# Performance work log

Hardware: AMD Instinct MI355X
Metric: run time of the kernel (lower is better)

The kernel has to match this reference:

```python
import jax, jax.numpy as jnp
import numpy as np

B, NQ, NK, DQ, DK, DV, H = 4, 512, 512, 512, 512, 512, 128
NEG_INF = -1e20


def setup_inputs() -> dict:
    key = jax.random.key(0)
    ks = jax.random.split(key, 7)
    Q = jax.random.normal(ks[0], (B, NQ, DQ), dtype=jnp.float32)
    K = jax.random.normal(ks[1], (B, NK, DK), dtype=jnp.float32)
    V = jax.random.normal(ks[2], (B, NK, DV), dtype=jnp.float32)
    # learned params (LazyLinear, bias=False): y = x @ W with W[in, out]
    Wq = jax.random.normal(ks[3], (DQ, H), dtype=jnp.float32) / np.sqrt(DQ)
    Wk = jax.random.normal(ks[4], (DK, H), dtype=jnp.float32) / np.sqrt(DK)
    wv = jax.random.normal(ks[5], (H,), dtype=jnp.float32) / np.sqrt(H)
    valid_lens = jax.random.randint(ks[6], (B,), 1, NK + 1).astype(jnp.int64)
    return {"Q": Q, "K": K, "V": V, "Wq": Wq, "Wk": Wk, "wv": wv,
            "valid_lens": valid_lens}


def reference(Q, K, V, Wq, Wk, wv, valid_lens):
    # Project queries and keys to shared hidden size H
    Qp = Q @ Wq                      # (B, NQ, H)
    Kp = K @ Wk                      # (B, NK, H)
    # Additive (Bahdanau) broadcast: (B, NQ, NK, H)
    S = jnp.tanh(Qp[:, :, None, :] + Kp[:, None, :, :])
    # Linear score to scalar: (B, NQ, NK)
    scores = jnp.einsum('bqkh,h->bqk', S, wv)
    # Mask positions k >= valid_lens[b] (1-D valid_lens broadcast over queries)
    kv_idx = jnp.arange(scores.shape[-1])[None, None, :]
    mask = kv_idx < valid_lens[:, None, None]
    scores = jnp.where(mask, scores, NEG_INF)
    W = jax.nn.softmax(scores, axis=-1)  # dropout rate 0.0 -> identity
    return jnp.einsum('bqk,bkv->bqv', W, V)
```

## Files before the change

### kernel.cpp

```cpp
#include <hip/hip_runtime.h>

#define B_   4
#define NQ_  512
#define NK_  512
#define D_   512
#define H_   128

typedef __attribute__((ext_vector_type(8))) short short8;
typedef __attribute__((ext_vector_type(4))) float f32x4;

__device__ __forceinline__ float fexp2(float x) { return __builtin_amdgcn_exp2f(x); }
__device__ __forceinline__ float frcp(float x)  { return __builtin_amdgcn_rcpf(x); }
__device__ __forceinline__ unsigned short f2bf(float f) {
    unsigned int u = __builtin_bit_cast(unsigned int, f);
    u += 0x7FFFu + ((u >> 16) & 1u);
    return (unsigned short)(u >> 16);
}

#define WS_QKP   0
#define WS_PP    524288
#define WS_WP    4718592
#define WS_WBF   4718848
#define WS_VT    5243136

__global__ __launch_bounds__(256) void proj_kernel(
    const float* __restrict__ Q, const float* __restrict__ K,
    const float* __restrict__ Wq, const float* __restrict__ Wk,
    float* __restrict__ Pp)
{
    const int xb = blockIdx.x;
    const int ks = blockIdx.y;
    const bool isQ = xb < 16;
    const float* __restrict__ X = isQ ? Q : K;
    const float* __restrict__ W = isQ ? Wq : Wk;
    const int r0 = (xb & 15) * 128;
    const int k0 = ks * 64;
    const int t  = threadIdx.x;

    __shared__ float At[32][132];
    __shared__ float Wl[32][132];

    const int cg = t & 15;
    const int rg = t >> 4;
    float acc[8][8] = {};

    for (int kc = 0; kc < 2; ++kc) {
        if (kc) __syncthreads();
        #pragma unroll
        for (int p = 0; p < 4; ++p) {
            const int idx = p * 256 + t;
            const int row = idx & 127;
            const int kq  = (idx >> 7) * 4;
            const float4 v = *reinterpret_cast<const float4*>(
                X + (size_t)(r0 + row) * D_ + k0 + kc * 32 + kq);
            At[kq + 0][row] = v.x; At[kq + 1][row] = v.y;
            At[kq + 2][row] = v.z; At[kq + 3][row] = v.w;
        }
        #pragma unroll
        for (int p = 0; p < 4; ++p) {
            const int idx = p * 256 + t;
            const int kr  = idx >> 5;
            const int c4  = (idx & 31) * 4;
            *reinterpret_cast<float4*>(&Wl[kr][c4]) =
                *reinterpret_cast<const float4*>(
                    W + (size_t)(k0 + kc * 32 + kr) * H_ + c4);
        }
        __syncthreads();

        #pragma unroll 4
        for (int k = 0; k < 32; ++k) {
            const float4 a0 = *reinterpret_cast<const float4*>(&At[k][rg * 8]);
            const float4 a1 = *reinterpret_cast<const float4*>(&At[k][rg * 8 + 4]);
            const float4 b0 = *reinterpret_cast<const float4*>(&Wl[k][cg * 4]);
            const float4 b1 = *reinterpret_cast<const float4*>(&Wl[k][64 + cg * 4]);
            const float aa[8] = {a0.x, a0.y, a0.z, a0.w, a1.x, a1.y, a1.z, a1.w};
            const float bb[8] = {b0.x, b0.y, b0.z, b0.w, b1.x, b1.y, b1.z, b1.w};
            #pragma unroll
            for (int r = 0; r < 8; ++r)
                #pragma unroll
                for (int c = 0; c < 8; ++c)
                    acc[r][c] = fmaf(aa[r], bb[c], acc[r][c]);
        }
    }

    float* __restrict__ dst = Pp + (size_t)ks * (4096 * 128);
    #pragma unroll
    for (int r = 0; r < 8; ++r) {
        const int grow = xb * 128 + rg * 8 + r;
        *reinterpret_cast<float4*>(dst + (size_t)grow * H_ + cg * 4) =
            make_float4(acc[r][0], acc[r][1], acc[r][2], acc[r][3]);
        *reinterpret_cast<float4*>(dst + (size_t)grow * H_ + 64 + cg * 4) =
            make_float4(acc[r][4], acc[r][5], acc[r][6], acc[r][7]);
    }
}

__global__ __launch_bounds__(256) void proj_add_kernel(
    const float* __restrict__ Pp, const float* __restrict__ wv,
    float* __restrict__ QKp, float* __restrict__ wp)
{
    const int i = blockIdx.x * 256 + threadIdx.x;
    const float C2 = 2.88539008177792681472f;
    float4 s = make_float4(0.f, 0.f, 0.f, 0.f);
    #pragma unroll
    for (int p = 0; p < 8; ++p) {
        const float4 v = reinterpret_cast<const float4*>(Pp)[(size_t)p * 131072 + i];
        s.x += v.x; s.y += v.y; s.z += v.z; s.w += v.w;
    }
    s.x *= C2; s.y *= C2; s.z *= C2; s.w *= C2;
    reinterpret_cast<float4*>(QKp)[i] = s;

    if (blockIdx.x == 0 && threadIdx.x < 64) {
        const float2 w2 = reinterpret_cast<const float2*>(wv)[threadIdx.x];
        const float wn0 = -2.0f * w2.x;
        const float wn1 = -2.0f * w2.y;
        reinterpret_cast<float4*>(wp)[threadIdx.x] =
            make_float4(wn0, wn1, wn0 + wn1, 0.0f);
    }
}

__global__ __launch_bounds__(256) void transposeV_kernel(
    const float* __restrict__ V, unsigned short* __restrict__ Vt)
{
    const int kt = blockIdx.x, dt = blockIdx.y, b = blockIdx.z;
    const int t  = threadIdx.x;
    __shared__ float Vl[64][69];

    #pragma unroll
    for (int p = 0; p < 4; ++p) {
        const int idx = p * 256 + t;
        const int r  = idx >> 4;
        const int c4 = (idx & 15) * 4;
        const float4 v = *reinterpret_cast<const float4*>(
            V + ((size_t)b * NK_ + kt * 64 + r) * D_ + dt * 64 + c4);
        Vl[r][c4 + 0] = v.x; Vl[r][c4 + 1] = v.y;
        Vl[r][c4 + 2] = v.z; Vl[r][c4 + 3] = v.w;
    }
    __syncthreads();

    #pragma unroll
    for (int p = 0; p < 4; ++p) {
        const int idx = p * 256 + t;
        const int d  = idx >> 4;
        const int k4 = (idx & 15) * 4;
        ushort4 o;
        o.x = f2bf(Vl[k4 + 0][d]); o.y = f2bf(Vl[k4 + 1][d]);
        o.z = f2bf(Vl[k4 + 2][d]); o.w = f2bf(Vl[k4 + 3][d]);
        *reinterpret_cast<ushort4*>(
            Vt + ((size_t)b * D_ + dt * 64 + d) * NK_ + kt * 64 + k4) = o;
    }
}

__global__ __launch_bounds__(512) void score_softmax_kernel(
    const float* __restrict__ QKp, const float* __restrict__ wp,
    const int* __restrict__ valid_lens, unsigned short* __restrict__ Wbf)
{
    const int b  = blockIdx.y;
    const int q0 = blockIdx.x * 8;
    const int t  = threadIdx.x;
    const int w    = __builtin_amdgcn_readfirstlane(t >> 6);
    const int lane = t & 63;

    __shared__ __align__(16) float4 Ks[64][33];

    const float4* __restrict__ Q4 =
        reinterpret_cast<const float4*>(QKp + (size_t)(b * NQ_ + q0 + w) * H_);
    const float4* __restrict__ wp4 = reinterpret_cast<const float4*>(wp);
    const float4* __restrict__ Kp4 =
        reinterpret_cast<const float4*>(QKp + (size_t)(2048 + b * NK_) * H_);

    float vals[8];

    for (int c = 0; c < 8; ++c) {
        if (c) __syncthreads();
        #pragma unroll
        for (int p = 0; p < 4; ++p) {
            const int idx = p * 512 + t;
            const int r   = idx >> 5;
            const int h4  = idx & 31;
            Ks[r][h4] = Kp4[(size_t)(c * 64 + r) * 32 + h4];
        }
        __syncthreads();

        float s = 0.0f;
        #pragma unroll 8
        for (int g = 0; g < 32; ++g) {
            const float4 kv = Ks[lane][g];
            const float4 qa = Q4[g];
            const float4 wa = wp4[2 * g];
            const float4 wb = wp4[2 * g + 1];
            const float e0 = fexp2(qa.x + kv.x);
            const float e1 = fexp2(qa.y + kv.y);
            const float e2 = fexp2(qa.z + kv.z);
            const float e3 = fexp2(qa.w + kv.w);
            float n0 = fmaf(wa.x, e1, wa.z); n0 = fmaf(wa.y, e0, n0);
            float n1 = fmaf(wb.x, e3, wb.z); n1 = fmaf(wb.y, e2, n1);
            const float d0 = (1.0f + e0) * (1.0f + e1);
            const float d1 = (1.0f + e2) * (1.0f + e3);
            s = fmaf(n0, frcp(d0), s);
            s = fmaf(n1, frcp(d1), s);
        }
        vals[c] = s;
    }

    const int vl = valid_lens[b];
    float m = -1e30f;
    #pragma unroll
    for (int c = 0; c < 8; ++c) {
        const int k = c * 64 + lane;
        vals[c] = (k < vl) ? vals[c] : -1e30f;
        m = fmaxf(m, vals[c]);
    }
    #pragma unroll
    for (int off = 32; off >= 1; off >>= 1)
        m = fmaxf(m, __shfl_xor(m, off, 64));

    const float L2E = 1.44269504088896340736f;
    float e[8];
    float sum = 0.0f;
    #pragma unroll
    for (int c = 0; c < 8; ++c) {
        e[c] = fexp2((vals[c] - m) * L2E);
        sum += e[c];
    }
    #pragma unroll
    for (int off = 32; off >= 1; off >>= 1)
        sum += __shfl_xor(sum, off, 64);

    const float inv = frcp(sum);
    unsigned short* __restrict__ dst = Wbf + (size_t)(b * NQ_ + q0 + w) * NK_;
    #pragma unroll
    for (int c = 0; c < 8; ++c)
        dst[c * 64 + lane] = f2bf(e[c] * inv);
}

__global__ __launch_bounds__(256) void av_gemm_kernel(
    const unsigned short* __restrict__ Wbf, const unsigned short* __restrict__ Vt,
    float* __restrict__ O)
{
    const int c0 = blockIdx.x * 64;
    const int r0 = blockIdx.y * 64;
    const int b  = blockIdx.z;
    const int t  = threadIdx.x;
    const int wave = __builtin_amdgcn_readfirstlane(t >> 6);
    const int lane = t & 63;
    const int m    = lane & 15;
    const int quad = lane >> 4;

    __shared__ unsigned short Al [64][136];
    __shared__ unsigned short Btl[64][136];

    f32x4 acc0 = {0.f,0.f,0.f,0.f}, acc1 = {0.f,0.f,0.f,0.f};
    f32x4 acc2 = {0.f,0.f,0.f,0.f}, acc3 = {0.f,0.f,0.f,0.f};

    for (int kc = 0; kc < 4; ++kc) {
        if (kc) __syncthreads();
        #pragma unroll
        for (int p = 0; p < 4; ++p) {
            const int idx = p * 256 + t;
            const int rl = idx >> 4;
            const int k8 = (idx & 15) * 8;
            *reinterpret_cast<uint4*>(&Al[rl][k8]) =
                *reinterpret_cast<const uint4*>(
                    Wbf + ((size_t)b * NQ_ + r0 + rl) * NK_ + kc * 128 + k8);
            *reinterpret_cast<uint4*>(&Btl[rl][k8]) =
                *reinterpret_cast<const uint4*>(
                    Vt + ((size_t)b * D_ + c0 + rl) * NK_ + kc * 128 + k8);
        }
        __syncthreads();

        #pragma unroll
        for (int sub = 0; sub < 4; ++sub) {
            const int kcol = sub * 32 + quad * 8;
            const short8 a = *reinterpret_cast<const short8*>(&Al[wave * 16 + m][kcol]);
            const short8 b0 = *reinterpret_cast<const short8*>(&Btl[ 0 + m][kcol]);
            const short8 b1 = *reinterpret_cast<const short8*>(&Btl[16 + m][kcol]);
            const short8 b2 = *reinterpret_cast<const short8*>(&Btl[32 + m][kcol]);
            const short8 b3 = *reinterpret_cast<const short8*>(&Btl[48 + m][kcol]);
            acc0 = __builtin_amdgcn_mfma_f32_16x16x32_bf16(a, b0, acc0, 0, 0, 0);
            acc1 = __builtin_amdgcn_mfma_f32_16x16x32_bf16(a, b1, acc1, 0, 0, 0);
            acc2 = __builtin_amdgcn_mfma_f32_16x16x32_bf16(a, b2, acc2, 0, 0, 0);
            acc3 = __builtin_amdgcn_mfma_f32_16x16x32_bf16(a, b3, acc3, 0, 0, 0);
        }
    }

    const size_t rowbase = (size_t)b * NQ_ + r0 + wave * 16 + quad * 4;
    #pragma unroll
    for (int i = 0; i < 4; ++i) {
        float* __restrict__ orow = O + (rowbase + i) * D_ + c0 + m;
        orow[ 0] = acc0[i];
        orow[16] = acc1[i];
        orow[32] = acc2[i];
        orow[48] = acc3[i];
    }
}

extern "C" void kernel_launch(void* const* d_in, const int* in_sizes, int n_in,
                              void* d_out, int out_size, void* d_ws, size_t ws_size,
                              hipStream_t stream) {
    (void)in_sizes; (void)n_in; (void)out_size; (void)ws_size;

    const float* Q   = (const float*)d_in[0];
    const float* K   = (const float*)d_in[1];
    const float* V   = (const float*)d_in[2];
    const float* Wq  = (const float*)d_in[3];
    const float* Wk  = (const float*)d_in[4];
    const float* wv  = (const float*)d_in[5];
    const int*   vl  = (const int*)d_in[6];
    float* out = (float*)d_out;

    float* ws  = (float*)d_ws;
    float* QKp = ws + WS_QKP;
    float* Pp  = ws + WS_PP;
    float* wp  = ws + WS_WP;
    unsigned short* Wbf = (unsigned short*)(ws + WS_WBF);
    unsigned short* Vt  = (unsigned short*)(ws + WS_VT);

    proj_kernel<<<dim3(32, 8), 256, 0, stream>>>(Q, K, Wq, Wk, Pp);
    proj_add_kernel<<<dim3(512), 256, 0, stream>>>(Pp, wv, QKp, wp);
    transposeV_kernel<<<dim3(8, 8, 4), 256, 0, stream>>>(V, Vt);
    score_softmax_kernel<<<dim3(64, 4), 512, 0, stream>>>(QKp, wp, vl, Wbf);
    av_gemm_kernel<<<dim3(8, 8, 4), 256, 0, stream>>>(Wbf, Vt, out);
}
```

Baseline: 131.4 us.

## Precompute exponentials of projections, merge V transpose into projection, split score rows

The projection-add stage now stores exp2 of the scaled projections, so the score loop replaces per-element exp2 with multiplies, using exp(a+b)=exp(a)exp(b) and one reciprocal per pair. The V transpose is folded into the projection kernel as extra blocks, removing one launch. The score kernel splits each query row across two waves (4 rows per block, 512 blocks) and combines the softmax max and sum through shared memory. This adds occupancy but risks overflow or precision loss when exp of large projections is multiplied.

```diff
diff --git a/kernel.cpp b/kernel.cpp
--- a/kernel.cpp
+++ b/kernel.cpp
@@ -17,86 +17,120 @@
     return (unsigned short)(u >> 16);
 }
 
-#define WS_QKP   0
+
+#define WS_EQK   0
 #define WS_PP    524288
 #define WS_WP    4718592
 #define WS_WBF   4718848
 #define WS_VT    5243136
 
-__global__ __launch_bounds__(256) void proj_kernel(
+__global__ __launch_bounds__(256) void prep_kernel(
     const float* __restrict__ Q, const float* __restrict__ K,
     const float* __restrict__ Wq, const float* __restrict__ Wk,
-    float* __restrict__ Pp)
+    const float* __restrict__ V,
+    float* __restrict__ Pp, unsigned short* __restrict__ Vt)
 {
-    const int xb = blockIdx.x;
-    const int ks = blockIdx.y;
-    const bool isQ = xb < 16;
-    const float* __restrict__ X = isQ ? Q : K;
-    const float* __restrict__ W = isQ ? Wq : Wk;
-    const int r0 = (xb & 15) * 128;
-    const int k0 = ks * 64;
-    const int t  = threadIdx.x;
-
-    __shared__ float At[32][132];
-    __shared__ float Wl[32][132];
-
-    const int cg = t & 15;
-    const int rg = t >> 4;
-    float acc[8][8] = {};
-
-    for (int kc = 0; kc < 2; ++kc) {
-        if (kc) __syncthreads();
+    __shared__ float smem[2 * 32 * 132];
+    const int t = threadIdx.x;
+
+    if (blockIdx.x < 32) {
+        const int xb = blockIdx.x;
+        const int ks = blockIdx.y;
+        const bool isQ = xb < 16;
+        const float* __restrict__ X = isQ ? Q : K;
+        const float* __restrict__ W = isQ ? Wq : Wk;
+        const int r0 = (xb & 15) * 128;
+        const int k0 = ks * 64;
+
+        float (*At)[132] = (float(*)[132])smem;
+        float (*Wl)[132] = (float(*)[132])(smem + 32 * 132);
+
+        const int cg = t & 15;
+        const int rg = t >> 4;
+        float acc[8][8] = {};
+
+        for (int kc = 0; kc < 2; ++kc) {
+            if (kc) __syncthreads();
+            #pragma unroll
+            for (int p = 0; p < 4; ++p) {
+                const int idx = p * 256 + t;
+                const int row = idx & 127;
+                const int kq  = (idx >> 7) * 4;
+                const float4 v = *reinterpret_cast<const float4*>(
+                    X + (size_t)(r0 + row) * D_ + k0 + kc * 32 + kq);
+                At[kq + 0][row] = v.x; At[kq + 1][row] = v.y;
+                At[kq + 2][row] = v.z; At[kq + 3][row] = v.w;
+            }
+            #pragma unroll
+            for (int p = 0; p < 4; ++p) {
+                const int idx = p * 256 + t;
+                const int kr  = idx >> 5;
+                const int c4  = (idx & 31) * 4;
+                *reinterpret_cast<float4*>(&Wl[kr][c4]) =
+                    *reinterpret_cast<const float4*>(
+                        W + (size_t)(k0 + kc * 32 + kr) * H_ + c4);
+            }
+            __syncthreads();
+
+            #pragma unroll 4
+            for (int k = 0; k < 32; ++k) {
+                const float4 a0 = *reinterpret_cast<const float4*>(&At[k][rg * 8]);
+                const float4 a1 = *reinterpret_cast<const float4*>(&At[k][rg * 8 + 4]);
+                const float4 b0 = *reinterpret_cast<const float4*>(&Wl[k][cg * 4]);
+                const float4 b1 = *reinterpret_cast<const float4*>(&Wl[k][64 + cg * 4]);
+                const float aa[8] = {a0.x, a0.y, a0.z, a0.w, a1.x, a1.y, a1.z, a1.w};
+                const float bb[8] = {b0.x, b0.y, b0.z, b0.w, b1.x, b1.y, b1.z, b1.w};
+                #pragma unroll
+                for (int r = 0; r < 8; ++r)
+                    #pragma unroll
+                    for (int c = 0; c < 8; ++c)
+                        acc[r][c] = fmaf(aa[r], bb[c], acc[r][c]);
+            }
+        }
+
+        float* __restrict__ dst = Pp + (size_t)blockIdx.y * (4096 * 128);
+        #pragma unroll
+        for (int r = 0; r < 8; ++r) {
+            const int grow = xb * 128 + rg * 8 + r;
+            *reinterpret_cast<float4*>(dst + (size_t)grow * H_ + cg * 4) =
+                make_float4(acc[r][0], acc[r][1], acc[r][2], acc[r][3]);
+            *reinterpret_cast<float4*>(dst + (size_t)grow * H_ + 64 + cg * 4) =
+                make_float4(acc[r][4], acc[r][5], acc[r][6], acc[r][7]);
+        }
+    } else {
+        const int id = (blockIdx.x - 32) * 8 + blockIdx.y;
+        const int kt = id & 7, dt = (id >> 3) & 7, b = id >> 6;
+        float (*Vl)[69] = (float(*)[69])smem;
+
         #pragma unroll
         for (int p = 0; p < 4; ++p) {
             const int idx = p * 256 + t;
-            const int row = idx & 127;
-            const int kq  = (idx >> 7) * 4;
+            const int r  = idx >> 4;
+            const int c4 = (idx & 15) * 4;
             const float4 v = *reinterpret_cast<const float4*>(
-                X + (size_t)(r0 + row) * D_ + k0 + kc * 32 + kq);
-            At[kq + 0][row] = v.x; At[kq + 1][row] = v.y;
-            At[kq + 2][row] = v.z; At[kq + 3][row] = v.w;
-        }
+                V + ((size_t)b * NK_ + kt * 64 + r) * D_ + dt * 64 + c4);
+            Vl[r][c4 + 0] = v.x; Vl[r][c4 + 1] = v.y;
+            Vl[r][c4 + 2] = v.z; Vl[r][c4 + 3] = v.w;
+        }
+        __syncthreads();
+
         #pragma unroll
         for (int p = 0; p < 4; ++p) {
             const int idx = p * 256 + t;
-            const int kr  = idx >> 5;
-            const int c4  = (idx & 31) * 4;
-            *reinterpret_cast<float4*>(&Wl[kr][c4]) =
-                *reinterpret_cast<const float4*>(
-                    W + (size_t)(k0 + kc * 32 + kr) * H_ + c4);
-        }
-        __syncthreads();
-
-        #pragma unroll 4
-        for (int k = 0; k < 32; ++k) {
-            const float4 a0 = *reinterpret_cast<const float4*>(&At[k][rg * 8]);
-            const float4 a1 = *reinterpret_cast<const float4*>(&At[k][rg * 8 + 4]);
-            const float4 b0 = *reinterpret_cast<const float4*>(&Wl[k][cg * 4]);
-            const float4 b1 = *reinterpret_cast<const float4*>(&Wl[k][64 + cg * 4]);
-            const float aa[8] = {a0.x, a0.y, a0.z, a0.w, a1.x, a1.y, a1.z, a1.w};
-            const float bb[8] = {b0.x, b0.y, b0.z, b0.w, b1.x, b1.y, b1.z, b1.w};
-            #pragma unroll
-            for (int r = 0; r < 8; ++r)
-                #pragma unroll
-                for (int c = 0; c < 8; ++c)
-                    acc[r][c] = fmaf(aa[r], bb[c], acc[r][c]);
-        }
-    }
-
-    float* __restrict__ dst = Pp + (size_t)ks * (4096 * 128);
-    #pragma unroll
-    for (int r = 0; r < 8; ++r) {
-        const int grow = xb * 128 + rg * 8 + r;
-        *reinterpret_cast<float4*>(dst + (size_t)grow * H_ + cg * 4) =
-            make_float4(acc[r][0], acc[r][1], acc[r][2], acc[r][3]);
-        *reinterpret_cast<float4*>(dst + (size_t)grow * H_ + 64 + cg * 4) =
-            make_float4(acc[r][4], acc[r][5], acc[r][6], acc[r][7]);
+            const int d  = idx >> 4;
+            const int k4 = (idx & 15) * 4;
+            ushort4 o;
+            o.x = f2bf(Vl[k4 + 0][d]); o.y = f2bf(Vl[k4 + 1][d]);
+            o.z = f2bf(Vl[k4 + 2][d]); o.w = f2bf(Vl[k4 + 3][d]);
+            *reinterpret_cast<ushort4*>(
+                Vt + ((size_t)b * D_ + dt * 64 + d) * NK_ + kt * 64 + k4) = o;
+        }
     }
 }
 
 __global__ __launch_bounds__(256) void proj_add_kernel(
     const float* __restrict__ Pp, const float* __restrict__ wv,
-    float* __restrict__ QKp, float* __restrict__ wp)
+    float* __restrict__ Eqk, float* __restrict__ wp)
 {
     const int i = blockIdx.x * 256 + threadIdx.x;
     const float C2 = 2.88539008177792681472f;
@@ -106,8 +140,9 @@
         const float4 v = reinterpret_cast<const float4*>(Pp)[(size_t)p * 131072 + i];
         s.x += v.x; s.y += v.y; s.z += v.z; s.w += v.w;
     }
-    s.x *= C2; s.y *= C2; s.z *= C2; s.w *= C2;
-    reinterpret_cast<float4*>(QKp)[i] = s;
+    s.x = fexp2(C2 * s.x); s.y = fexp2(C2 * s.y);
+    s.z = fexp2(C2 * s.z); s.w = fexp2(C2 * s.w);
+    reinterpret_cast<float4*>(Eqk)[i] = s;
 
     if (blockIdx.x == 0 && threadIdx.x < 64) {
         const float2 w2 = reinterpret_cast<const float2*>(wv)[threadIdx.x];
@@ -118,119 +153,98 @@
     }
 }
 
-__global__ __launch_bounds__(256) void transposeV_kernel(
-    const float* __restrict__ V, unsigned short* __restrict__ Vt)
-{
-    const int kt = blockIdx.x, dt = blockIdx.y, b = blockIdx.z;
-    const int t  = threadIdx.x;
-    __shared__ float Vl[64][69];
-
-    #pragma unroll
-    for (int p = 0; p < 4; ++p) {
-        const int idx = p * 256 + t;
-        const int r  = idx >> 4;
-        const int c4 = (idx & 15) * 4;
-        const float4 v = *reinterpret_cast<const float4*>(
-            V + ((size_t)b * NK_ + kt * 64 + r) * D_ + dt * 64 + c4);
-        Vl[r][c4 + 0] = v.x; Vl[r][c4 + 1] = v.y;
-        Vl[r][c4 + 2] = v.z; Vl[r][c4 + 3] = v.w;
-    }
-    __syncthreads();
-
-    #pragma unroll
-    for (int p = 0; p < 4; ++p) {
-        const int idx = p * 256 + t;
-        const int d  = idx >> 4;
-        const int k4 = (idx & 15) * 4;
-        ushort4 o;
-        o.x = f2bf(Vl[k4 + 0][d]); o.y = f2bf(Vl[k4 + 1][d]);
-        o.z = f2bf(Vl[k4 + 2][d]); o.w = f2bf(Vl[k4 + 3][d]);
-        *reinterpret_cast<ushort4*>(
-            Vt + ((size_t)b * D_ + dt * 64 + d) * NK_ + kt * 64 + k4) = o;
-    }
-}
-
-__global__ __launch_bounds__(512) void score_softmax_kernel(
-    const float* __restrict__ QKp, const float* __restrict__ wp,
+__global__ __launch_bounds__(512, 4) void score_softmax_kernel(
+    const float* __restrict__ Eqk, const float* __restrict__ wp,
     const int* __restrict__ valid_lens, unsigned short* __restrict__ Wbf)
 {
-    const int b  = blockIdx.y;
-    const int q0 = blockIdx.x * 8;
-    const int t  = threadIdx.x;
+    const int rb   = blockIdx.x;
+    const int t    = threadIdx.x;
     const int w    = __builtin_amdgcn_readfirstlane(t >> 6);
     const int lane = t & 63;
-
-    __shared__ __align__(16) float4 Ks[64][33];
+    const int rloc = w >> 1;
+    const int half = w & 1;
+    const int row  = rb * 4 + rloc;
+    const int b    = row >> 9;
+
+    __shared__ __align__(16) float4 Ks[2 * 64 * 33];
+    __shared__ float redM[4][2], redS[4][2];
 
     const float4* __restrict__ Q4 =
-        reinterpret_cast<const float4*>(QKp + (size_t)(b * NQ_ + q0 + w) * H_);
+        reinterpret_cast<const float4*>(Eqk + (size_t)row * H_);
     const float4* __restrict__ wp4 = reinterpret_cast<const float4*>(wp);
     const float4* __restrict__ Kp4 =
-        reinterpret_cast<const float4*>(QKp + (size_t)(2048 + b * NK_) * H_);
-
-    float vals[8];
-
-    for (int c = 0; c < 8; ++c) {
+        reinterpret_cast<const float4*>(Eqk + (size_t)(2048 + b * NK_) * H_);
+
+    float vals[4];
+
+    for (int c = 0; c < 4; ++c) {
         if (c) __syncthreads();
         #pragma unroll
-        for (int p = 0; p < 4; ++p) {
+        for (int p = 0; p < 8; ++p) {
             const int idx = p * 512 + t;
-            const int r   = idx >> 5;
+            const int hh  = idx >> 11;
+            const int r   = (idx >> 5) & 63;
             const int h4  = idx & 31;
-            Ks[r][h4] = Kp4[(size_t)(c * 64 + r) * 32 + h4];
+            Ks[(hh * 64 + r) * 33 + h4] =
+                Kp4[(size_t)(hh * 256 + c * 64 + r) * 32 + h4];
         }
         __syncthreads();
 
         float s = 0.0f;
-        #pragma unroll 8
+        #pragma unroll 4
         for (int g = 0; g < 32; ++g) {
-            const float4 kv = Ks[lane][g];
+            const float4 kv = Ks[(half * 64 + lane) * 33 + g];
             const float4 qa = Q4[g];
             const float4 wa = wp4[2 * g];
             const float4 wb = wp4[2 * g + 1];
-            const float e0 = fexp2(qa.x + kv.x);
-            const float e1 = fexp2(qa.y + kv.y);
-            const float e2 = fexp2(qa.z + kv.z);
-            const float e3 = fexp2(qa.w + kv.w);
-            float n0 = fmaf(wa.x, e1, wa.z); n0 = fmaf(wa.y, e0, n0);
-            float n1 = fmaf(wb.x, e3, wb.z); n1 = fmaf(wb.y, e2, n1);
-            const float d0 = (1.0f + e0) * (1.0f + e1);
-            const float d1 = (1.0f + e2) * (1.0f + e3);
-            s = fmaf(n0, frcp(d0), s);
-            s = fmaf(n1, frcp(d1), s);
+            const float e0 = qa.x * kv.x;
+            const float e1 = qa.y * kv.y;
+            const float e2 = qa.z * kv.z;
+            const float e3 = qa.w * kv.w;
+            const float D01 = 1.0f + fmaf(e0, e1, e0 + e1);
+            const float D23 = 1.0f + fmaf(e2, e3, e2 + e3);
+            const float n01 = fmaf(wa.y, e0, fmaf(wa.x, e1, wa.z));
+            const float n23 = fmaf(wb.y, e2, fmaf(wb.x, e3, wb.z));
+            const float N   = fmaf(n23, D01, n01 * D23);
+            s = fmaf(N, frcp(D01 * D23), s);
         }
         vals[c] = s;
     }
 
     const int vl = valid_lens[b];
+    const float L2E = 1.44269504088896340736f;
     float m = -1e30f;
     #pragma unroll
-    for (int c = 0; c < 8; ++c) {
-        const int k = c * 64 + lane;
+    for (int c = 0; c < 4; ++c) {
+        const int k = half * 256 + c * 64 + lane;
         vals[c] = (k < vl) ? vals[c] : -1e30f;
         m = fmaxf(m, vals[c]);
     }
     #pragma unroll
     for (int off = 32; off >= 1; off >>= 1)
         m = fmaxf(m, __shfl_xor(m, off, 64));
-
-    const float L2E = 1.44269504088896340736f;
-    float e[8];
     float sum = 0.0f;
     #pragma unroll
-    for (int c = 0; c < 8; ++c) {
-        e[c] = fexp2((vals[c] - m) * L2E);
-        sum += e[c];
-    }
+    for (int c = 0; c < 4; ++c)
+        sum += fexp2((vals[c] - m) * L2E);
     #pragma unroll
     for (int off = 32; off >= 1; off >>= 1)
         sum += __shfl_xor(sum, off, 64);
 
-    const float inv = frcp(sum);
-    unsigned short* __restrict__ dst = Wbf + (size_t)(b * NQ_ + q0 + w) * NK_;
-    #pragma unroll
-    for (int c = 0; c < 8; ++c)
-        dst[c * 64 + lane] = f2bf(e[c] * inv);
+    if (lane == 0) { redM[rloc][half] = m; redS[rloc][half] = sum; }
+    __syncthreads();
+
+    const float m0 = redM[rloc][0], m1 = redM[rloc][1];
+    const float s0 = redS[rloc][0], s1 = redS[rloc][1];
+    const float M  = fmaxf(m0, m1);
+    const float S  = fmaf(s0, fexp2((m0 - M) * L2E),
+                          s1 * fexp2((m1 - M) * L2E));
+    const float inv = frcp(S);
+
+    unsigned short* __restrict__ dst = Wbf + (size_t)row * NK_ + half * 256;
+    #pragma unroll
+    for (int c = 0; c < 4; ++c)
+        dst[c * 64 + lane] = f2bf(fexp2((vals[c] - M) * L2E) * inv);
 }
 
 __global__ __launch_bounds__(256) void av_gemm_kernel(
@@ -309,15 +323,14 @@
     float* out = (float*)d_out;
 
     float* ws  = (float*)d_ws;
-    float* QKp = ws + WS_QKP;
+    float* Eqk = ws + WS_EQK;
     float* Pp  = ws + WS_PP;
     float* wp  = ws + WS_WP;
     unsigned short* Wbf = (unsigned short*)(ws + WS_WBF);
     unsigned short* Vt  = (unsigned short*)(ws + WS_VT);
 
-    proj_kernel<<<dim3(32, 8), 256, 0, stream>>>(Q, K, Wq, Wk, Pp);
-    proj_add_kernel<<<dim3(512), 256, 0, stream>>>(Pp, wv, QKp, wp);
-    transposeV_kernel<<<dim3(8, 8, 4), 256, 0, stream>>>(V, Vt);
-    score_softmax_kernel<<<dim3(64, 4), 512, 0, stream>>>(QKp, wp, vl, Wbf);
+    prep_kernel<<<dim3(64, 8), 256, 0, stream>>>(Q, K, Wq, Wk, V, Pp, Vt);
+    proj_add_kernel<<<dim3(512), 256, 0, stream>>>(Pp, wv, Eqk, wp);
+    score_softmax_kernel<<<dim3(512), 512, 0, stream>>>(Eqk, wp, vl, Wbf);
     av_gemm_kernel<<<dim3(8, 8, 4), 256, 0, stream>>>(Wbf, Vt, out);
 }
```

Result: faster. 121.4 us (-7.6%).
